# Kernel tuning notes

Hardware: AMD Instinct MI355X
Metric: run time of the kernel (lower is better)

The kernel has to match this reference:

```python
import jax, jax.numpy as jnp
import numpy as np

B, S, D, H = 2, 2048, 2048, 16
DH = D // H
EPS = 1e-5


def layernorm(x, gamma, beta):
    mu = jnp.mean(x, axis=-1, keepdims=True)
    var = jnp.var(x, axis=-1, keepdims=True)
    return (x - mu) * jax.lax.rsqrt(var + EPS) * gamma + beta


def setup_inputs() -> dict:
    key = jax.random.key(0)
    ks = jax.random.split(key, 10)
    sc = 1.0 / np.sqrt(D)
    return {
        "x": jax.random.normal(ks[0], (B, S, D), dtype=jnp.float32),
        "wq": jax.random.normal(ks[1], (D, D), dtype=jnp.float32) * sc,
        "bq": jnp.zeros((D,), jnp.float32),
        "wk": jax.random.normal(ks[2], (D, D), dtype=jnp.float32) * sc,
        "bk": jnp.zeros((D,), jnp.float32),
        "wv": jax.random.normal(ks[3], (D, D), dtype=jnp.float32) * sc,
        "bv": jnp.zeros((D,), jnp.float32),
        "wf": jax.random.normal(ks[4], (D, D), dtype=jnp.float32) * sc,
        "bf": jnp.zeros((D,), jnp.float32),
        "gamma": jnp.ones((D,), jnp.float32),
        "beta": jnp.zeros((D,), jnp.float32),
    }


def reference(x, wq, bq, wk, bk, wv, bv, wf, bf, gamma, beta):
    q = x @ wq + bq
    k = x @ wk + bk
    v = x @ wv + bv
    # split: [B,S,D] -> [B,H,S,DH]
    split = lambda t: t.reshape(B, S, H, DH).transpose(0, 2, 1, 3)
    q, k, v = split(q), split(k), split(v)
    s = jnp.einsum("bhqd,bhkd->bhqk", q, k) / np.sqrt(DH)
    p = jax.nn.softmax(s, axis=-1)
    o = jnp.einsum("bhqk,bhkd->bhqd", p, v)
    # faithful to original buggy concat: flat view of [B,H,S,DH] as [B,S,H*DH]
    o = o.reshape(B, S, H * DH)
    vb = o
    h1 = layernorm(o + x, gamma, beta)
    h2 = h1 @ wf + bf
    out = layernorm(h2 + vb, gamma, beta)
    return out
```

## Files before the change

kernel.cpp:

```cpp
#include <hip/hip_runtime.h>


#define B_ 2
#define S_ 2048
#define D_ 2048
#define H_ 16
#define DH_ 128

typedef __attribute__((ext_vector_type(8))) short s16x8;
typedef __attribute__((ext_vector_type(8))) unsigned short u16x8;
typedef __attribute__((ext_vector_type(4))) float f32x4;
typedef __attribute__((ext_vector_type(4))) unsigned short u16x4;

#define MFMA16(a, b, c) __builtin_amdgcn_mfma_f32_16x16x32_bf16(a, b, c, 0, 0, 0)

__device__ inline unsigned short f2bf(float f) {
  union { float f; unsigned u; } x; x.f = f;
  unsigned r = (x.u + 0x7fffu + ((x.u >> 16) & 1u)) >> 16;
  return (unsigned short)r;
}
__device__ inline float bf2f(unsigned short u) {
  union { unsigned u; float f; } x; x.u = ((unsigned)u) << 16;
  return x.f;
}
__device__ inline unsigned pack2bf(float a, float b) {
  unsigned ua = __builtin_bit_cast(unsigned, a) + 0x8000u;
  unsigned ub = __builtin_bit_cast(unsigned, b) + 0x8000u;
  return __builtin_amdgcn_perm(ub, ua, 0x07060302u);
}

__device__ inline void gld_lds16(const void* g, void* l) {
  __builtin_amdgcn_global_load_lds(
      (__attribute__((address_space(1))) void*)g,
      (__attribute__((address_space(3))) void*)l, 16, 0, 0);
}

__global__ __launch_bounds__(256) void prep_kernel(
    const float* __restrict__ x, unsigned short* __restrict__ xb,
    const float* __restrict__ w0, const float* __restrict__ w1,
    const float* __restrict__ w2, const float* __restrict__ w3,
    unsigned short* __restrict__ o0, unsigned short* __restrict__ o1,
    unsigned short* __restrict__ o2, unsigned short* __restrict__ o3) {
  int z = blockIdx.z;
  int t = threadIdx.x;
  if (z == 4) {
    int base = (blockIdx.y * 32 + blockIdx.x) * 16384 + t * 4;
#pragma unroll
    for (int p = 0; p < 16; ++p) {
      int i = base + p * 1024;
      float4 v = *(const float4*)&x[i];
      u16x4 o;
      o.x = f2bf(v.x); o.y = f2bf(v.y); o.z = f2bf(v.z); o.w = f2bf(v.w);
      *(u16x4*)&xb[i] = o;
    }
    return;
  }
  __shared__ short Ts[64 * 136];
  const float* W = z == 0 ? w0 : z == 1 ? w1 : z == 2 ? w2 : w3;
  unsigned short* WT = z == 0 ? o0 : z == 1 ? o1 : z == 2 ? o2 : o3;
  int n0 = blockIdx.x * 64, k0 = blockIdx.y * 128;
  int cl = t & 15, rw = t >> 4;
  int kb = k0 + rw * 8, nb = n0 + cl * 4;
  float4 f[8];
#pragma unroll
  for (int r = 0; r < 8; ++r) f[r] = *(const float4*)&W[(kb + r) * D_ + nb];
#define TPOSE(comp, i)                                                      \
  {                                                                         \
    u16x8 o = {f2bf(f[0].comp), f2bf(f[1].comp), f2bf(f[2].comp),           \
               f2bf(f[3].comp), f2bf(f[4].comp), f2bf(f[5].comp),           \
               f2bf(f[6].comp), f2bf(f[7].comp)};                           \
    *(u16x8*)&Ts[(cl * 4 + i) * 136 + rw * 8] = o;                          \
  }
  TPOSE(x, 0) TPOSE(y, 1) TPOSE(z, 2) TPOSE(w, 3)
#undef TPOSE
  __syncthreads();
#pragma unroll
  for (int p = 0; p < 4; ++p) {
    int e = t + 256 * p;
    int n = e >> 4, kc = e & 15;
    u16x8 o = *(const u16x8*)&Ts[n * 136 + kc * 8];
    *(u16x8*)&WT[(n0 + n) * D_ + k0 + kc * 8] = o;
  }
}

template <int QKV>
__global__ __launch_bounds__(512, 1) void gemm8p_kernel(
    const unsigned short* __restrict__ A, const unsigned short* __restrict__ W0,
    const unsigned short* __restrict__ W1, const unsigned short* __restrict__ W2,
    const float* __restrict__ b0, const float* __restrict__ b1,
    const float* __restrict__ b2, unsigned short* __restrict__ Qb,
    unsigned short* __restrict__ Kb, unsigned short* __restrict__ Vt,
    float qscale) {
  __shared__ short As3[3][256 * 64];
  __shared__ short Bs3[3][128 * 64];
  int idx = blockIdx.x;
  const int nwg = QKV ? 768 : 256;
  const int cpx = nwg >> 3;
  int wg = (idx & 7) * cpx + (idx >> 3);
  int wi, mt, ntile;
  if (QKV) {
    wi = wg >> 8;
    int rem = wg & 255;
    mt = rem >> 4; ntile = rem & 15;
  } else {
    wi = 0; mt = wg >> 4; ntile = wg & 15;
  }
  int m0 = mt * 256, n0 = ntile * 128;
  const unsigned short* BT = QKV ? (wi == 0 ? W0 : wi == 1 ? W1 : W2) : W0;
  const float* bias = QKV ? (wi == 0 ? b0 : wi == 1 ? b1 : b2) : b0;
  float oscale = (QKV && wi == 0) ? qscale : 1.0f;

  int t = threadIdx.x, lane = t & 63, w = t >> 6;
  int nl = lane & 15, q = lane >> 4;
  int wr = (w >> 1) * 64, wc = (w & 1) * 64;
  int swz = nl & 7;

  int aoff[4], boff[2], aldst[4], bldst[2];
#pragma unroll
  for (int l = 0; l < 4; ++l) {
    int e = t + 512 * l;
    int row = e >> 3, c = e & 7;
    aoff[l] = (m0 + row) * 2048 + (c ^ (row & 7)) * 8;
    aldst[l] = e * 8;
  }
#pragma unroll
  for (int l = 0; l < 2; ++l) {
    int e = t + 512 * l;
    int row = e >> 3, c = e & 7;
    boff[l] = (n0 + row) * 2048 + (c ^ (row & 7)) * 8;
    bldst[l] = e * 8;
  }

  f32x4 acc[4][4];
  f32x4 z4 = {0.f, 0.f, 0.f, 0.f};
#pragma unroll
  for (int i = 0; i < 4; ++i)
#pragma unroll
    for (int j = 0; j < 4; ++j) acc[i][j] = z4;

#pragma unroll
  for (int kt = 0; kt < 2; ++kt) {
#pragma unroll
    for (int l = 0; l < 4; ++l)
      gld_lds16(&A[aoff[l] + kt * 64], &As3[kt][aldst[l]]);
#pragma unroll
    for (int l = 0; l < 2; ++l)
      gld_lds16(&BT[boff[l] + kt * 64], &Bs3[kt][bldst[l]]);
  }
  asm volatile("s_waitcnt vmcnt(6)" ::: "memory");
  __builtin_amdgcn_s_barrier();

  int scur = 0;
  for (int kt = 0; kt < 32; ++kt) {
    const short* Asl = As3[scur];
    const short* Bsl = Bs3[scur];
    int sn = scur + 2; if (sn >= 3) sn -= 3;
    short* Ad = As3[sn];
    short* Bd = Bs3[sn];
    int kst = (kt + 2) * 64;
    bool st = kt < 30;
    s16x8 af[4], bf[4];
#pragma unroll
    for (int i = 0; i < 4; ++i)
      af[i] = *(const s16x8*)&Asl[(wr + i * 16 + nl) * 64 + (q ^ swz) * 8];
#pragma unroll
    for (int j = 0; j < 4; ++j)
      bf[j] = *(const s16x8*)&Bsl[(wc + j * 16 + nl) * 64 + (q ^ swz) * 8];
    if (st) {
      gld_lds16(&A[aoff[0] + kst], &Ad[aldst[0]]);
      gld_lds16(&A[aoff[1] + kst], &Ad[aldst[1]]);
      gld_lds16(&BT[boff[0] + kst], &Bd[bldst[0]]);
    }
    __builtin_amdgcn_s_setprio(1);
#pragma unroll
    for (int i = 0; i < 4; ++i)
#pragma unroll
      for (int j = 0; j < 4; ++j) acc[i][j] = MFMA16(af[i], bf[j], acc[i][j]);
    __builtin_amdgcn_s_setprio(0);
#pragma unroll
    for (int i = 0; i < 4; ++i)
      af[i] = *(const s16x8*)&Asl[(wr + i * 16 + nl) * 64 + ((4 + q) ^ swz) * 8];
#pragma unroll
    for (int j = 0; j < 4; ++j)
      bf[j] = *(const s16x8*)&Bsl[(wc + j * 16 + nl) * 64 + ((4 + q) ^ swz) * 8];
    if (st) {
      gld_lds16(&A[aoff[2] + kst], &Ad[aldst[2]]);
      gld_lds16(&A[aoff[3] + kst], &Ad[aldst[3]]);
      gld_lds16(&BT[boff[1] + kst], &Bd[bldst[1]]);
    }
    __builtin_amdgcn_s_setprio(1);
#pragma unroll
    for (int i = 0; i < 4; ++i)
#pragma unroll
      for (int j = 0; j < 4; ++j) acc[i][j] = MFMA16(af[i], bf[j], acc[i][j]);
    __builtin_amdgcn_s_setprio(0);
    if (kt < 31) {
      if (st)
        asm volatile("s_waitcnt vmcnt(6)" ::: "memory");
      else
        asm volatile("s_waitcnt vmcnt(0)" ::: "memory");
      __builtin_amdgcn_s_barrier();
    }
    scur = scur + 1; if (scur == 3) scur = 0;
  }

#pragma unroll
  for (int i = 0; i < 4; ++i)
#pragma unroll
    for (int j = 0; j < 4; ++j) {
      int row = m0 + wr + i * 16 + q * 4;
      int col = n0 + wc + j * 16 + nl;
      float bv = bias[col];
      float v[4];
#pragma unroll
      for (int r = 0; r < 4; ++r) v[r] = (acc[i][j][r] + bv) * oscale;
      if (QKV && wi == 2) {
        unsigned d0 = pack2bf(v[0], v[1]), d1 = pack2bf(v[2], v[3]);
        long idxv = ((long)(((row >> 11) * 16 + (col >> 7)) * 128 + (col & 127))) * 2048 +
                    (row & 2047);
        *(uint2*)&Vt[idxv] = (uint2){d0, d1};
      } else {
        unsigned short* out = (QKV && wi == 1) ? Kb : Qb;
#pragma unroll
        for (int r = 0; r < 4; ++r)
          out[(row + r) * 2048 + col] = f2bf(v[r]);
      }
    }
}

__global__ __launch_bounds__(512, 1) void attn_kernel(
    const unsigned short* __restrict__ Q, const unsigned short* __restrict__ K,
    const unsigned short* __restrict__ VT, unsigned short* __restrict__ O) {
  __shared__ short KsA[8192], KsB[8192];
  __shared__ short VsA[8192], VsB[8192];
  __shared__ short Ps[16384];
  int t = threadIdx.x, lane = t & 63, w = t >> 6;
  int nl = lane & 15, q = lane >> 4;
  int i = blockIdx.x;
  int xcd = i & 7, j = i >> 3;
  int bh = xcd + 8 * (j & 3);
  int qb = j >> 2;
  int b = bh >> 4, h = bh & 15;

  s16x8 qf[2][4];
  int qrow = b * S_ + qb * 256 + w * 32;
#pragma unroll
  for (int t2 = 0; t2 < 2; ++t2)
#pragma unroll
    for (int kc = 0; kc < 4; ++kc)
      qf[t2][kc] = *(const s16x8*)&Q[(qrow + t2 * 16 + nl) * D_ + h * DH_ + kc * 32 + q * 8];

  f32x4 z4 = {0.f, 0.f, 0.f, 0.f};
  f32x4 accO[2][8];
  f32x4 l4[2] = {z4, z4};
#pragma unroll
  for (int t2 = 0; t2 < 2; ++t2)
#pragma unroll
    for (int n8 = 0; n8 < 8; ++n8) accO[t2][n8] = z4;

  int swz = nl & 7;

  const unsigned short* kp[2];
  const unsigned short* vp[2];
#pragma unroll
  for (int i2 = 0; i2 < 2; ++i2) {
    int c = t + 512 * i2;
    int s = c >> 4, p = c & 15;
    kp[i2] = K + (long)(b * S_ + s) * D_ + h * DH_ + ((p ^ (s & 7)) * 8);
    int d = c >> 3, cp = c & 7, cs = cp ^ (d & 7);
    vp[i2] = VT + (long)(bh * DH_ + d) * S_ + cs * 8;
  }

#define STAGE(bufK, bufV)                           \
  {                                                 \
    _Pragma("unroll") for (int i2 = 0; i2 < 2; ++i2) { \
      gld_lds16(kp[i2], &bufK[(t + 512 * i2) * 8]); \
      gld_lds16(vp[i2], &bufV[(t + 512 * i2) * 8]); \
      kp[i2] += 64 * D_;                            \
      vp[i2] += 64;                                 \
    }                                               \
  }

  auto compute = [&](const short* Ks, const short* Vs) {
    f32x4 accS[2][4];
#pragma unroll
    for (int t2 = 0; t2 < 2; ++t2)
#pragma unroll
      for (int n = 0; n < 4; ++n) accS[t2][n] = z4;
    __builtin_amdgcn_s_setprio(1);
#pragma unroll
    for (int kc = 0; kc < 4; ++kc) {
      s16x8 kf[4];
#pragma unroll
      for (int n = 0; n < 4; ++n)
        kf[n] = *(const s16x8*)&Ks[(n * 16 + nl) * 128 +
                                   ((((kc << 2) + q) ^ swz)) * 8];
#pragma unroll
      for (int t2 = 0; t2 < 2; ++t2)
#pragma unroll
        for (int n = 0; n < 4; ++n)
          accS[t2][n] = MFMA16(kf[n], qf[t2][kc], accS[t2][n]);
    }
    __builtin_amdgcn_s_setprio(0);

#pragma unroll
    for (int t2 = 0; t2 < 2; ++t2) {
      int prow = (w * 32 + t2 * 16 + nl) * 64;
#pragma unroll
      for (int n = 0; n < 4; ++n) {
#pragma unroll
        for (int r = 0; r < 4; ++r)
          accS[t2][n][r] = __builtin_amdgcn_exp2f(accS[t2][n][r] - 16.0f);
        l4[t2] += accS[t2][n];
        unsigned d0 = pack2bf(accS[t2][n][0], accS[t2][n][1]);
        unsigned d1 = pack2bf(accS[t2][n][2], accS[t2][n][3]);
        int c8 = q + 4 * n;
        int off = prow + (((c8 >> 1) ^ swz) * 8 + (c8 & 1) * 4);
        *(uint2*)&Ps[off] = (uint2){d0, d1};
      }
    }

    __builtin_amdgcn_s_setprio(1);
#pragma unroll
    for (int ks = 0; ks < 2; ++ks) {
      s16x8 pf[2];
#pragma unroll
      for (int t2 = 0; t2 < 2; ++t2)
        pf[t2] = *(const s16x8*)&Ps[(w * 32 + t2 * 16 + nl) * 64 + ((4 * ks + q) ^ swz) * 8];
#pragma unroll
      for (int n8 = 0; n8 < 8; ++n8) {
        int d = n8 * 16 + nl;
        int cs = ks * 4 + q;
        int ci = d * 8 + (cs ^ (d & 7));
        s16x8 vf = *(const s16x8*)&Vs[ci * 8];
#pragma unroll
        for (int t2 = 0; t2 < 2; ++t2)
          accO[t2][n8] = MFMA16(vf, pf[t2], accO[t2][n8]);
      }
    }
    __builtin_amdgcn_s_setprio(0);
  };

  STAGE(KsA, VsA);
  for (int it = 0; it < 32; it += 2) {
    __syncthreads();
    STAGE(KsB, VsB);
    compute(KsA, VsA);
    __syncthreads();
    if (it + 2 < 32) STAGE(KsA, VsA);
    compute(KsB, VsB);
  }
#undef STAGE

#pragma unroll
  for (int t2 = 0; t2 < 2; ++t2) {
    float l = (l4[t2][0] + l4[t2][1]) + (l4[t2][2] + l4[t2][3]);
    l += __shfl_xor(l, 16);
    l += __shfl_xor(l, 32);
    float inv = 1.0f / l;
    int s = qb * 256 + w * 32 + t2 * 16 + nl;
    unsigned short* orow = &O[((long)(bh * S_ + s)) * DH_];
#pragma unroll
    for (int n8 = 0; n8 < 8; ++n8) {
      unsigned d0 = pack2bf(accO[t2][n8][0] * inv, accO[t2][n8][1] * inv);
      unsigned d1 = pack2bf(accO[t2][n8][2] * inv, accO[t2][n8][3] * inv);
      *(uint2*)&orow[n8 * 16 + q * 4] = (uint2){d0, d1};
    }
  }
}

template <int OUTBF, int INBF>
__global__ __launch_bounds__(256) void ln_kernel(
    const void* __restrict__ Ain, const unsigned short* __restrict__ Ob,
    const float* __restrict__ gamma, const float* __restrict__ beta,
    void* __restrict__ out) {
  int row = blockIdx.x, t = threadIdx.x;
  int lane = t & 63, w = t >> 6;
  int c0 = t * 8;
  float v[8], s = 0.f, s2 = 0.f;
  u16x8 ob = *(const u16x8*)&Ob[row * D_ + c0];
  if (INBF) {
    u16x8 a = *(const u16x8*)&((const unsigned short*)Ain)[row * D_ + c0];
#pragma unroll
    for (int p = 0; p < 8; ++p) v[p] = bf2f(a[p]);
  } else {
    float4 a0 = *(const float4*)&((const float*)Ain)[row * D_ + c0];
    float4 a1 = *(const float4*)&((const float*)Ain)[row * D_ + c0 + 4];
    v[0] = a0.x; v[1] = a0.y; v[2] = a0.z; v[3] = a0.w;
    v[4] = a1.x; v[5] = a1.y; v[6] = a1.z; v[7] = a1.w;
  }
#pragma unroll
  for (int p = 0; p < 8; ++p) {
    v[p] += bf2f(ob[p]);
    s += v[p]; s2 += v[p] * v[p];
  }
#pragma unroll
  for (int mk = 32; mk >= 1; mk >>= 1) {
    s += __shfl_xor(s, mk);
    s2 += __shfl_xor(s2, mk);
  }
  __shared__ float red[8];
  if (lane == 0) { red[w * 2] = s; red[w * 2 + 1] = s2; }
  __syncthreads();
  s = red[0] + red[2] + red[4] + red[6];
  s2 = red[1] + red[3] + red[5] + red[7];
  float mu = s * (1.0f / D_);
  float var = s2 * (1.0f / D_) - mu * mu;
  float rs = rsqrtf(var + 1e-5f);
  float4 g0 = *(const float4*)&gamma[c0], g1 = *(const float4*)&gamma[c0 + 4];
  float4 b0 = *(const float4*)&beta[c0], b1 = *(const float4*)&beta[c0 + 4];
  float g[8] = {g0.x, g0.y, g0.z, g0.w, g1.x, g1.y, g1.z, g1.w};
  float bb[8] = {b0.x, b0.y, b0.z, b0.w, b1.x, b1.y, b1.z, b1.w};
  float o[8];
#pragma unroll
  for (int p = 0; p < 8; ++p) o[p] = (v[p] - mu) * rs * g[p] + bb[p];
  if (OUTBF) {
    u16x8 ov;
#pragma unroll
    for (int p = 0; p < 8; ++p) ov[p] = f2bf(o[p]);
    *(u16x8*)&((unsigned short*)out)[row * D_ + c0] = ov;
  } else {
    float4 o0 = {o[0], o[1], o[2], o[3]}, o1 = {o[4], o[5], o[6], o[7]};
    *(float4*)&((float*)out)[row * D_ + c0] = o0;
    *(float4*)&((float*)out)[row * D_ + c0 + 4] = o1;
  }
}

extern "C" void kernel_launch(void* const* d_in, const int* in_sizes, int n_in,
                              void* d_out, int out_size, void* d_ws, size_t ws_size,
                              hipStream_t stream) {
  const float* x     = (const float*)d_in[0];
  const float* wq    = (const float*)d_in[1];
  const float* bq    = (const float*)d_in[2];
  const float* wk    = (const float*)d_in[3];
  const float* bk    = (const float*)d_in[4];
  const float* wv    = (const float*)d_in[5];
  const float* bv    = (const float*)d_in[6];
  const float* wf    = (const float*)d_in[7];
  const float* bfb   = (const float*)d_in[8];
  const float* gamma = (const float*)d_in[9];
  const float* beta  = (const float*)d_in[10];

  unsigned short* ws  = (unsigned short*)d_ws;
  unsigned short* WqT = ws;
  unsigned short* WkT = ws + 4194304;
  unsigned short* WvT = ws + 8388608;
  unsigned short* WfT = ws + 12582912;
  unsigned short* Xb  = ws + 16777216;
  unsigned short* Qb  = ws + 25165824;
  unsigned short* Kb  = ws + 33554432;
  unsigned short* Vt  = ws + 41943040;
  unsigned short* Ob  = Xb;
  unsigned short* H1  = Kb;
  unsigned short* H2b = Vt;

  const float scl2 = 0.08838834764831845f * 1.4426950408889634f;

  dim3 blk(256);
  prep_kernel<<<dim3(32, 16, 5), blk, 0, stream>>>(
      x, Xb, wq, wk, wv, wf, WqT, WkT, WvT, WfT);

  gemm8p_kernel<1><<<dim3(768), dim3(512), 0, stream>>>(
      Xb, WqT, WkT, WvT, bq, bk, bv, Qb, Kb, Vt, scl2);

  attn_kernel<<<dim3(256), dim3(512), 0, stream>>>(Qb, Kb, Vt, Ob);

  ln_kernel<1, 0><<<dim3(4096), blk, 0, stream>>>(x, Ob, gamma, beta, (void*)H1);
  gemm8p_kernel<0><<<dim3(256), dim3(512), 0, stream>>>(
      H1, WfT, WfT, WfT, bfb, bfb, bfb, H2b, H2b, H2b, 1.0f);
  ln_kernel<0, 1><<<dim3(4096), blk, 0, stream>>>(H2b, Ob, gamma, beta, d_out);
}
```

Measured before the change: 380.8 us.

## Triple-buffer K/V tiles in attention with partial vmcnt waits

Replaces the double-buffered K/V LDS staging in the attention kernel with a three-slot ring that keeps two tiles in flight. Partial s_waitcnt vmcnt(4) waits plus a raw barrier replace __syncthreads, so a compute step only waits for the oldest load. The aim is to hide global-to-LDS latency better. It costs 32KB more LDS, and correctness depends on the hand-counted vmcnt values and on the compute loop's own Ps barriers.

```diff
diff --git a/kernel.cpp b/kernel.cpp
--- a/kernel.cpp
+++ b/kernel.cpp
@@ -231,8 +231,8 @@
 __global__ __launch_bounds__(512, 1) void attn_kernel(
     const unsigned short* __restrict__ Q, const unsigned short* __restrict__ K,
     const unsigned short* __restrict__ VT, unsigned short* __restrict__ O) {
-  __shared__ short KsA[8192], KsB[8192];
-  __shared__ short VsA[8192], VsB[8192];
+  __shared__ short Ks3[3][8192];
+  __shared__ short Vs3[3][8192];
   __shared__ short Ps[16384];
   int t = threadIdx.x, lane = t & 63, w = t >> 6;
   int nl = lane & 15, q = lane >> 4;
@@ -271,14 +271,14 @@
     vp[i2] = VT + (long)(bh * DH_ + d) * S_ + cs * 8;
   }
 
-#define STAGE(bufK, bufV)                           \
-  {                                                 \
-    _Pragma("unroll") for (int i2 = 0; i2 < 2; ++i2) { \
-      gld_lds16(kp[i2], &bufK[(t + 512 * i2) * 8]); \
-      gld_lds16(vp[i2], &bufV[(t + 512 * i2) * 8]); \
-      kp[i2] += 64 * D_;                            \
-      vp[i2] += 64;                                 \
-    }                                               \
+#define STAGE(slot)                                      \
+  {                                                      \
+    _Pragma("unroll") for (int i2 = 0; i2 < 2; ++i2) {   \
+      gld_lds16(kp[i2], &Ks3[slot][(t + 512 * i2) * 8]); \
+      gld_lds16(vp[i2], &Vs3[slot][(t + 512 * i2) * 8]); \
+      kp[i2] += 64 * D_;                                 \
+      vp[i2] += 64;                                      \
+    }                                                    \
   }
 
   auto compute = [&](const short* Ks, const short* Vs) {
@@ -341,14 +341,24 @@
     __builtin_amdgcn_s_setprio(0);
   };
 
-  STAGE(KsA, VsA);
-  for (int it = 0; it < 32; it += 2) {
-    __syncthreads();
-    STAGE(KsB, VsB);
-    compute(KsA, VsA);
-    __syncthreads();
-    if (it + 2 < 32) STAGE(KsA, VsA);
-    compute(KsB, VsB);
+  STAGE(0);
+  STAGE(1);
+  asm volatile("s_waitcnt vmcnt(4)" ::: "memory");
+  __builtin_amdgcn_s_barrier();
+
+  int scur = 0;
+  for (int kt = 0; kt < 32; ++kt) {
+    int sn = scur + 2; if (sn >= 3) sn -= 3;
+    if (kt < 30) STAGE(sn);
+    compute(Ks3[scur], Vs3[scur]);
+    if (kt < 31) {
+      if (kt < 30)
+        asm volatile("s_waitcnt vmcnt(4)" ::: "memory");
+      else
+        asm volatile("s_waitcnt vmcnt(0)" ::: "memory");
+      __builtin_amdgcn_s_barrier();
+    }
+    scur = scur + 1; if (scur == 3) scur = 0;
   }
 #undef STAGE
 
```

Measured after the change: 395.7 us. 3.9% more time.
